# Optimization experiments

Measured on AMD Instinct MI355X. Metric: run time of the kernel, lower is better.

Reference implementation:

```python
import jax, jax.numpy as jnp
import numpy as np


def setup_inputs() -> dict:
    key = jax.random.key(0)
    kD, kx, kc = jax.random.split(key, 3)
    B, N, I, O = 8, 20000, 64, 64
    KM = 8 * 32  # k_bands * m_samples = 256
    D = jax.random.normal(kD, (B, N, KM), dtype=jnp.float32)
    x = jax.random.normal(kx, (B, N, I), dtype=jnp.float32)
    coefficients = jax.random.normal(kc, (1, O, I, KM), dtype=jnp.float32)
    return {"D": D, "x": x, "coefficients": coefficients}


def reference(D, x, coefficients):
    # D: (B, N, M), x: (B, N, I), coefficients: (1, O, I, M)
    # Original: C = diag_embed(coeff) -> (1,O,I,M,M); einsum('boimj,bomi->boij')
    # Since C is diagonal in (m, j), that einsum is an elementwise scale:
    #   C_Dt_x[b,o,i,m] = coeff[o,i,m] * Dt_x[b,m,i]
    # and the final contraction + channel-sum is:
    #   out[b,n,o] = (1/sqrt(M)) * sum_m D[b,n,m] * sum_i coeff[o,i,m] * Dt_x[b,m,i]
    M = D.shape[2]
    coeff = coefficients[0]                              # (O, I, M)
    Dt_x = jnp.einsum('bnm,bni->bmi', D, x)              # (B, M, I)
    S = jnp.einsum('oim,bmi->bom', coeff, Dt_x)          # (B, O, M)
    out = jnp.einsum('bnm,bom->bno', D, S) / jnp.sqrt(jnp.asarray(M, D.dtype))
    return out  # (B, N, O)
```

## Files before the change

### kernel.cpp

```cpp
#include <hip/hip_runtime.h>

#define B 8
#define N 20000
#define M 256
#define I 64
#define O 64
#define MI (M * I)
#define KT 32
#define SSS 264
#define MSW(m) ((m) ^ (((m) >> 3) & 7))

typedef __attribute__((ext_vector_type(8))) short   bf16x8;
typedef __attribute__((ext_vector_type(4))) float   f32x4;
typedef __attribute__((ext_vector_type(4))) unsigned int uint4v;

__device__ __forceinline__ unsigned pk2bf(float lo, float hi) {
    unsigned a = __float_as_uint(lo);
    unsigned b = __float_as_uint(hi);
    a = (a + 0x7fffu + ((a >> 16) & 1u)) >> 16;
    b = (b + 0x7fffu + ((b >> 16) & 1u)) >> 16;
    return a | (b << 16);
}

__device__ __forceinline__ unsigned short f2bf(float v) {
    unsigned a = __float_as_uint(v);
    return (unsigned short)((a + 0x7fffu + ((a >> 16) & 1u)) >> 16);
}

__global__ __launch_bounds__(256) void stage1(const float* __restrict__ Dg,
                                              const float* __restrict__ xg,
                                              float* __restrict__ partial,
                                              int chunk) {
    const int b = blockIdx.y, s = blockIdx.x;
    const int n0 = s * chunk;
    const int nend = min(n0 + chunk, N);
    const int tid = threadIdx.x;
    const int lane = tid & 63;
    const int w = tid >> 6;

    __shared__ unsigned short sD[2][4 * 256 * 8];
    __shared__ unsigned short sX[2][4 * 64 * 8];

    f32x4 acc[4][4];
#pragma unroll
    for (int a = 0; a < 4; ++a)
#pragma unroll
        for (int v = 0; v < 4; ++v) acc[a][v] = (f32x4){0.f, 0.f, 0.f, 0.f};

    const float* Db = Dg + (size_t)b * N * M;
    const float* xb = xg + (size_t)b * N * I;

    const int steps = (nend > n0) ? (nend - n0 + KT - 1) / KT : 0;

    float4 dreg[8];
    float  xreg[8];

    if (steps > 0) {
#pragma unroll
        for (int q = 0; q < 8; ++q) {
            const int nc = min(n0 + w * 8 + q, N - 1);
            dreg[q] = *(const float4*)&Db[(size_t)nc * M + lane * 4];
            xreg[q] = xb[(size_t)nc * I + lane];
        }

        for (int t = 0; t < steps; ++t) {
            const int nb = n0 + t * KT;
            const int cur = t & 1;
#pragma unroll
            for (int q = 0; q < 8; ++q) {
                const bool valid = (nb + w * 8 + q) < nend;
                if (!valid) { dreg[q] = make_float4(0.f, 0.f, 0.f, 0.f); xreg[q] = 0.f; }
            }
#pragma unroll
            for (int j = 0; j < 4; ++j) {
                uint4v cell;
#pragma unroll
                for (int e = 0; e < 4; ++e)
                    cell[e] = pk2bf(((const float*)&dreg[2 * e])[j],
                                    ((const float*)&dreg[2 * e + 1])[j]);
                const int m = lane * 4 + j;
                *(uint4v*)&sD[cur][((size_t)w * 256 + MSW(m)) * 8] = cell;
            }
            {
                uint4v cell;
#pragma unroll
                for (int e = 0; e < 4; ++e)
                    cell[e] = pk2bf(xreg[2 * e], xreg[2 * e + 1]);
                *(uint4v*)&sX[cur][((size_t)w * 64 + lane) * 8] = cell;
            }
            if (t + 1 < steps) {
                const int nb2 = nb + KT;
#pragma unroll
                for (int q = 0; q < 8; ++q) {
                    const int nc = min(nb2 + w * 8 + q, N - 1);
                    dreg[q] = *(const float4*)&Db[(size_t)nc * M + lane * 4];
                    xreg[q] = xb[(size_t)nc * I + lane];
                }
            }
            __syncthreads();
            const int g = lane >> 4;
            bf16x8 bfr[4];
#pragma unroll
            for (int v = 0; v < 4; ++v)
                bfr[v] = *(const bf16x8*)&sX[cur][((size_t)g * 64 + v * 16 + (lane & 15)) * 8];
#pragma unroll
            for (int sm = 0; sm < 4; ++sm) {
                const int mm = w * 64 + sm * 16 + (lane & 15);
                bf16x8 afr = *(const bf16x8*)&sD[cur][((size_t)g * 256 + MSW(mm)) * 8];
#pragma unroll
                for (int v = 0; v < 4; ++v)
                    acc[sm][v] = __builtin_amdgcn_mfma_f32_16x16x32_bf16(
                        afr, bfr[v], acc[sm][v], 0, 0, 0);
            }
        }
    }

    float* p = partial + ((size_t)s * B + b) * MI;
#pragma unroll
    for (int sm = 0; sm < 4; ++sm)
#pragma unroll
        for (int v = 0; v < 4; ++v)
#pragma unroll
            for (int r = 0; r < 4; ++r) {
                const int m = w * 64 + sm * 16 + ((lane >> 4) << 2) + r;
                const int i = v * 16 + (lane & 15);
                p[m * I + i] = acc[sm][v][r];
            }
}

__global__ __launch_bounds__(256) void reduce_partials(const float* __restrict__ partial,
                                                       float* __restrict__ dtx,
                                                       int nsplit) {
    const int bb = blockIdx.y;
    const int j = blockIdx.x * 256 + threadIdx.x;
    const float* p = partial + (size_t)bb * MI + j;
    float sum = 0.f;
#pragma unroll 4
    for (int s = 0; s < nsplit; ++s)
        sum += p[(size_t)s * B * MI];
    dtx[(size_t)bb * MI + j] = sum;
}

__global__ __launch_bounds__(256) void stage2(const float* __restrict__ coeff,
                                              const float* __restrict__ dtx,
                                              unsigned short* __restrict__ ST) {
    const int g = blockIdx.x * 256 + threadIdx.x;
    const int b = g >> 14;
    const int rem = g & 16383;
    const int o = rem >> 8;
    const int m = rem & 255;
    const float* dt = dtx + (size_t)b * MI + (size_t)m * I;
    const float* cf = coeff + (size_t)o * I * M + m;
    float acc = 0.f;
#pragma unroll 8
    for (int i = 0; i < I; ++i)
        acc = fmaf(cf[(size_t)i * M], dt[i], acc);
    ST[((size_t)b * O + o) * M + m] = f2bf(acc * 0.0625f);
}

__global__ __launch_bounds__(256) void stage3(const float* __restrict__ Dg,
                                              const unsigned short* __restrict__ STg,
                                              float* __restrict__ outg) {
    const int b = blockIdx.y;
    const int n0 = blockIdx.x * 256;
    const int tid = threadIdx.x;
    const int lane = tid & 63;
    const int w = tid >> 6;

    __shared__ unsigned short sS[64 * SSS];

    {
        const int o = tid >> 2, seg = (tid & 3) * 64;
        const unsigned short* src = STg + ((size_t)b * O + o) * M + seg;
        unsigned short* dst = &sS[o * SSS + seg];
#pragma unroll
        for (int c = 0; c < 8; ++c)
            *(uint4v*)&dst[c * 8] = *(const uint4v*)&src[c * 8];
    }

    f32x4 acc[4][4];
#pragma unroll
    for (int a = 0; a < 4; ++a)
#pragma unroll
        for (int v = 0; v < 4; ++v) acc[a][v] = (f32x4){0.f, 0.f, 0.f, 0.f};

    __syncthreads();

    const float* Db = Dg + (size_t)b * N * M;
    const int k8 = (lane >> 4) << 3;

#pragma unroll 1
    for (int ks = 0; ks < 8; ++ks) {
        const int kb = ks * 32 + k8;
        bf16x8 bfr[4];
#pragma unroll
        for (int v = 0; v < 4; ++v)
            bfr[v] = *(const bf16x8*)&sS[(v * 16 + (lane & 15)) * SSS + kb];
#pragma unroll
        for (int sn = 0; sn < 4; ++sn) {
            int n = n0 + w * 64 + sn * 16 + (lane & 15);
            n = min(n, N - 1);
            const float* ap = Db + (size_t)n * M + kb;
            const float4 f0 = *(const float4*)ap;
            const float4 f1 = *(const float4*)(ap + 4);
            uint4v pk = {pk2bf(f0.x, f0.y), pk2bf(f0.z, f0.w),
                         pk2bf(f1.x, f1.y), pk2bf(f1.z, f1.w)};
            bf16x8 afr = __builtin_bit_cast(bf16x8, pk);
#pragma unroll
            for (int v = 0; v < 4; ++v)
                acc[sn][v] = __builtin_amdgcn_mfma_f32_16x16x32_bf16(
                    afr, bfr[v], acc[sn][v], 0, 0, 0);
        }
    }

#pragma unroll
    for (int sn = 0; sn < 4; ++sn)
#pragma unroll
        for (int v = 0; v < 4; ++v)
#pragma unroll
            for (int r = 0; r < 4; ++r) {
                const int n = n0 + w * 64 + sn * 16 + ((lane >> 4) << 2) + r;
                if (n < N)
                    outg[((size_t)b * N + n) * O + v * 16 + (lane & 15)] = acc[sn][v][r];
            }
}

extern "C" void kernel_launch(void* const* d_in, const int* in_sizes, int n_in,
                              void* d_out, int out_size, void* d_ws, size_t ws_size,
                              hipStream_t stream) {
    const float* Dg    = (const float*)d_in[0];
    const float* xg    = (const float*)d_in[1];
    const float* coeff = (const float*)d_in[2];
    float* outg = (float*)d_out;

    float* base = (float*)d_ws;
    float* dtx = base;
    unsigned short* ST = (unsigned short*)(base + B * MI);
    float* partial = base + B * MI + B * MI / 2;

    const size_t fixed = (size_t)B * MI * 4 + (size_t)B * MI * 2;
    const size_t per   = (size_t)B * MI * sizeof(float);
    int split = 1;
    if (ws_size > fixed) {
        size_t cap = (ws_size - fixed) / per;
        split = (int)(cap < 1 ? 1 : (cap > 64 ? 64 : cap));
    }
    int chunk = ((N + split - 1) / split + KT - 1) & ~(KT - 1);

    stage1<<<dim3(split, B), 256, 0, stream>>>(Dg, xg, partial, chunk);
    reduce_partials<<<dim3(MI / 256, B), 256, 0, stream>>>(partial, dtx, split);
    stage2<<<dim3((B * O * M) / 256), 256, 0, stream>>>(coeff, dtx, ST);
    stage3<<<dim3((N + 255) / 256, B), 256, 0, stream>>>(Dg, ST, outg);
}
```

Before: 101.4 us.

## Use hardware bf16 pack, add unclamped interior load path, raise split cap

Replaces the software round-to-nearest bf16 packing with the v_cvt_pk_bf16_f32 instruction. Adds a fast path for interior chunks that drops the per-row clamp and zero masking, cutting address arithmetic in the stage1 load loop. Raises the maximum N-split from 64 to 96 so more blocks run in stage1. The extra partial sums make the reduce kernel do more work, and rounding of special values may differ slightly from the software conversion.

```diff
diff --git a/kernel.cpp b/kernel.cpp
--- a/kernel.cpp
+++ b/kernel.cpp
@@ -15,11 +15,9 @@
 typedef __attribute__((ext_vector_type(4))) unsigned int uint4v;
 
 __device__ __forceinline__ unsigned pk2bf(float lo, float hi) {
-    unsigned a = __float_as_uint(lo);
-    unsigned b = __float_as_uint(hi);
-    a = (a + 0x7fffu + ((a >> 16) & 1u)) >> 16;
-    b = (b + 0x7fffu + ((b >> 16) & 1u)) >> 16;
-    return a | (b << 16);
+    unsigned r;
+    asm("v_cvt_pk_bf16_f32 %0, %1, %2" : "=v"(r) : "v"(lo), "v"(hi));
+    return r;
 }
 
 __device__ __forceinline__ unsigned short f2bf(float v) {
@@ -37,6 +35,7 @@
     const int tid = threadIdx.x;
     const int lane = tid & 63;
     const int w = tid >> 6;
+    const bool interior = (n0 + chunk) <= N;
 
     __shared__ unsigned short sD[2][4 * 256 * 8];
     __shared__ unsigned short sX[2][4 * 64 * 8];
@@ -55,21 +54,37 @@
     float4 dreg[8];
     float  xreg[8];
 
-    if (steps > 0) {
+    auto load_fast = [&](int nbase) {
+        const float* dp = &Db[(size_t)(nbase + w * 8) * M + lane * 4];
+        const float* xp = &xb[(size_t)(nbase + w * 8) * I + lane];
 #pragma unroll
         for (int q = 0; q < 8; ++q) {
-            const int nc = min(n0 + w * 8 + q, N - 1);
+            dreg[q] = *(const float4*)(dp + (size_t)q * M);
+            xreg[q] = xp[(size_t)q * I];
+        }
+    };
+    auto load_clamped = [&](int nbase) {
+#pragma unroll
+        for (int q = 0; q < 8; ++q) {
+            const int nc = min(nbase + w * 8 + q, N - 1);
             dreg[q] = *(const float4*)&Db[(size_t)nc * M + lane * 4];
             xreg[q] = xb[(size_t)nc * I + lane];
         }
+    };
+
+    if (steps > 0) {
+        if (interior) load_fast(n0); else load_clamped(n0);
 
         for (int t = 0; t < steps; ++t) {
             const int nb = n0 + t * KT;
             const int cur = t & 1;
-#pragma unroll
-            for (int q = 0; q < 8; ++q) {
-                const bool valid = (nb + w * 8 + q) < nend;
-                if (!valid) { dreg[q] = make_float4(0.f, 0.f, 0.f, 0.f); xreg[q] = 0.f; }
+            if (!interior) {
+#pragma unroll
+                for (int q = 0; q < 8; ++q)
+                    if (nb + w * 8 + q >= nend) {
+                        dreg[q] = make_float4(0.f, 0.f, 0.f, 0.f);
+                        xreg[q] = 0.f;
+                    }
             }
 #pragma unroll
             for (int j = 0; j < 4; ++j) {
@@ -89,13 +104,7 @@
                 *(uint4v*)&sX[cur][((size_t)w * 64 + lane) * 8] = cell;
             }
             if (t + 1 < steps) {
-                const int nb2 = nb + KT;
-#pragma unroll
-                for (int q = 0; q < 8; ++q) {
-                    const int nc = min(nb2 + w * 8 + q, N - 1);
-                    dreg[q] = *(const float4*)&Db[(size_t)nc * M + lane * 4];
-                    xreg[q] = xb[(size_t)nc * I + lane];
-                }
+                if (interior) load_fast(nb + KT); else load_clamped(nb + KT);
             }
             __syncthreads();
             const int g = lane >> 4;
@@ -243,7 +252,7 @@
     int split = 1;
     if (ws_size > fixed) {
         size_t cap = (ws_size - fixed) / per;
-        split = (int)(cap < 1 ? 1 : (cap > 64 ? 64 : cap));
+        split = (int)(cap < 1 ? 1 : (cap > 96 ? 96 : cap));
     }
     int chunk = ((N + split - 1) / split + KT - 1) & ~(KT - 1);
 
```

Result: slower. 106.1 us (+4.6%).
